# Kernel optimization log

Hardware: AMD Instinct MI355X
Metric: run time of the kernel (lower is better)

The kernel has to match this reference:

```python
import jax, jax.numpy as jnp
import numpy as np
import math

B, S, D, H, M = 2, 2048, 1024, 16, 64
HD = D // H  # head_dim = 64


def setup_inputs() -> dict:
    key = jax.random.key(0)
    ks = jax.random.split(key, 16)
    inp = {
        "query": jax.random.normal(ks[0], (B, S, D), jnp.float32),
        "key": jax.random.normal(ks[1], (B, S, D), jnp.float32),
        "value": jax.random.normal(ks[2], (B, S, D), jnp.float32),
        "mask": jax.random.randint(ks[3], (B, 1, 1, S), 0, 2, jnp.int32),
        "Wq": jax.random.normal(ks[4], (D, D), jnp.float32) * 0.02,
        "bq": jnp.zeros((D,), jnp.float32),
        "Wk": jax.random.normal(ks[5], (D, D), jnp.float32) * 0.02,
        "bk": jnp.zeros((D,), jnp.float32),
        "Wv": jax.random.normal(ks[6], (D, D), jnp.float32) * 0.02,
        "bv": jnp.zeros((D,), jnp.float32),
        "Wo": jax.random.normal(ks[7], (D, D), jnp.float32) * 0.02,
        "bo": jnp.zeros((D,), jnp.float32),
        "m_k": jax.random.normal(ks[8], (1, M, D), jnp.float32) * (1.0 / HD),
        "m_v": jax.random.normal(ks[9], (1, M, D), jnp.float32) * (1.0 / M),
    }
    return inp


def reference(query, key, value, mask, Wq, bq, Wk, bk, Wv, bv, Wo, bo, m_k, m_v):
    b, nq, d = query.shape
    nk = key.shape[1]
    h, hd, m = H, HD, M
    scale = math.sqrt(hd)

    Q = query @ Wq.T + bq                      # [b, nq, d]
    K = key @ Wk.T + bk                        # [b, nk, d]
    V = value @ Wv.T + bv                      # [b, nk, d]

    mk = scale * jnp.broadcast_to(m_k, (b, m, d))           # sqrt(head_dim)*m_k
    mv = math.sqrt(m) * jnp.broadcast_to(m_v, (b, m, d))    # sqrt(m)*m_v

    K = jnp.concatenate([K, mk], axis=1)       # [b, nk+m, d]
    V = jnp.concatenate([V, mv], axis=1)

    Qh = Q.reshape(b, nq, h, hd).transpose(0, 2, 1, 3)           # [b,h,nq,hd]
    Kh = K.reshape(b, nk + m, h, hd).transpose(0, 2, 1, 3)       # [b,h,nk+m,hd]
    Vh = V.reshape(b, nk + m, h, hd).transpose(0, 2, 1, 3)

    energy = jnp.einsum('bhqd,bhkd->bhqk', Qh, Kh) / scale       # [b,h,nq,nk+m]
    # mask only the first nk key columns; memory slots are never masked
    masked = jnp.where(mask == 0, jnp.float32(-1e20), energy[..., :nk])
    energy = jnp.concatenate([masked, energy[..., nk:]], axis=-1)

    attention = jax.nn.softmax(energy, axis=-1)
    x = jnp.einsum('bhqk,bhkd->bhqd', attention, Vh)             # [b,h,nq,hd]
    x = x.transpose(0, 2, 1, 3).reshape(b, nq, d)
    return x @ Wo.T + bo
```

## Files before the change

kernel.cpp:

```cpp
#include <hip/hip_runtime.h>
#include <hip/hip_bf16.h>
#include <stdint.h>

#define B_  2
#define S_  2048
#define D_  1024
#define H_  16
#define HD_ 64
#define M_  64
#define SKM (S_ + M_)
#define LOG2E 1.44269504088896340736f

typedef __attribute__((ext_vector_type(8))) short s16x8;
typedef __attribute__((ext_vector_type(4))) float f32x4;
typedef __attribute__((ext_vector_type(16))) float f32x16;

#define GLOAD16(gp, lp) __builtin_amdgcn_global_load_lds( \
    (const __attribute__((address_space(1))) void*)(gp),  \
    (__attribute__((address_space(3))) void*)(lp), 16, 0, 0)

#define WAITVM4() do { asm volatile("s_waitcnt vmcnt(4)" ::: "memory"); \
                       __builtin_amdgcn_sched_barrier(0); } while (0)
#define WAITVM0() do { asm volatile("s_waitcnt vmcnt(0)" ::: "memory"); \
                       __builtin_amdgcn_sched_barrier(0); } while (0)
#define BARRIER() do { asm volatile("" ::: "memory"); \
                       __builtin_amdgcn_s_barrier(); \
                       asm volatile("" ::: "memory"); } while (0)

__device__ __forceinline__ unsigned short f2bf(float f) {
  union { float f; unsigned int u; } v; v.f = f;
  unsigned int r = v.u + 0x7fffu + ((v.u >> 16) & 1u);
  return (unsigned short)(r >> 16);
}

__device__ __forceinline__ unsigned pkbf(float lo, float hi) {
  union { __hip_bfloat162 b; unsigned u; } t;
  t.b = __float22bfloat162_rn(make_float2(lo, hi));
  return t.u;
}

__global__ void compact_mask(const int* __restrict__ mask,
                             int* __restrict__ idx, int* __restrict__ cnt) {
  const int b = blockIdx.x;
  __shared__ int base, wsum[4];
  if (threadIdx.x == 0) base = 0;
  const int lane = threadIdx.x & 63, w = threadIdx.x >> 6;
  __syncthreads();
  for (int c = 0; c < S_; c += 256) {
    int key = c + threadIdx.x;
    int mv = mask[b * S_ + key];
    unsigned long long bal = __ballot(mv != 0);
    int pre = __popcll(bal & ((1ull << lane) - 1ull));
    if (lane == 0) wsum[w] = __popcll(bal);
    __syncthreads();
    int woff = 0;
    for (int i = 0; i < w; i++) woff += wsum[i];
    int tot = wsum[0] + wsum[1] + wsum[2] + wsum[3];
    if (mv) idx[b * S_ + base + woff + pre] = key;
    __syncthreads();
    if (threadIdx.x == 0) base += tot;
    __syncthreads();
  }
  if (threadIdx.x == 0) cnt[b] = base;
}

__global__ void cvt_f32_to_bf16(const float* __restrict__ in,
                                unsigned short* __restrict__ out) {
  int i = (blockIdx.x * blockDim.x + threadIdx.x) * 4;
  float4 v = *(const float4*)&in[i];
  ushort4 o;
  o.x = f2bf(v.x); o.y = f2bf(v.y); o.z = f2bf(v.z); o.w = f2bf(v.w);
  *(ushort4*)&out[i] = o;
}

__global__ void cvt_w4(const float* __restrict__ w0, const float* __restrict__ w1,
                       const float* __restrict__ w2, const float* __restrict__ w3,
                       unsigned short* __restrict__ o0, unsigned short* __restrict__ o1,
                       unsigned short* __restrict__ o2, unsigned short* __restrict__ o3) {
  const float* in; unsigned short* out;
  switch (blockIdx.y) {
    case 0: in = w0; out = o0; break;
    case 1: in = w1; out = o1; break;
    case 2: in = w2; out = o2; break;
    default: in = w3; out = o3; break;
  }
  int i = (blockIdx.x * 256 + threadIdx.x) * 4;
  float4 v = *(const float4*)&in[i];
  ushort4 o;
  o.x = f2bf(v.x); o.y = f2bf(v.y); o.z = f2bf(v.z); o.w = f2bf(v.w);
  *(ushort4*)&out[i] = o;
}

__global__ void cvt_kv_gather(const float* __restrict__ key, const float* __restrict__ value,
                              unsigned short* __restrict__ kf, unsigned short* __restrict__ vf,
                              const int* __restrict__ idx, const int* __restrict__ cnt) {
  int b = blockIdx.y, j = blockIdx.x;
  if (j >= cnt[b]) return;
  const float* in = blockIdx.z ? value : key;
  unsigned short* out = blockIdx.z ? vf : kf;
  int src = idx[b * S_ + j];
  const float* ip = in + ((size_t)(b * S_) + src) * D_;
  unsigned short* op = out + ((size_t)(b * S_) + j) * D_;
  int t = threadIdx.x * 4;
  float4 v = *(const float4*)&ip[t];
  ushort4 o;
  o.x = f2bf(v.x); o.y = f2bf(v.y); o.z = f2bf(v.z); o.w = f2bf(v.w);
  *(ushort4*)&op[t] = o;
}

__global__ void fill_mem(const float* __restrict__ mk, const float* __restrict__ mv,
                         unsigned short* __restrict__ Kb, unsigned short* __restrict__ VtG,
                         const int* __restrict__ cnt) {
  int i = blockIdx.x * 256 + threadIdx.x;
  int row = i >> 10, col = i & 1023;
  int hI = col >> 6, dd = col & 63;
  unsigned short kv = f2bf(8.0f * mk[i]);
  unsigned short vv = f2bf(8.0f * mv[i]);
#pragma unroll
  for (int b = 0; b < B_; b++) {
    int c = cnt[b];
    Kb[((size_t)(b * SKM) + c + row) * D_ + col] = kv;
    VtG[((size_t)(b * H_ + hI) * HD_ + dd) * SKM + c + row] = vv;
  }
}

__device__ __forceinline__ void gemm_core2(
    const unsigned short* __restrict__ A,
    const unsigned short* __restrict__ Bw,
    unsigned short* As, unsigned short* Bs,
    int mBase, int nBase, int K,
    int w, int lane, int wr, int wc, int lr, int lk,
    f32x4 acc[4][4]) {
  const int srow = w * 32 + (lane >> 2);
  const int cd = lane & 3;
  const int NT = K / 32;

#define STAGE_(buf, k0)                                                          \
  {                                                                              \
    _Pragma("unroll")                                                            \
    for (int i = 0; i < 2; i++) {                                                \
      int r = srow + i * 16;                                                     \
      int ca = cd ^ ((r >> 1) & 3);           \
      GLOAD16(&A[(size_t)(mBase + r) * K + (k0) + ca * 8],                       \
              &As[(buf) * (128 * 32) + (w * 32 + i * 16) * 32]);                 \
      GLOAD16(&Bw[(size_t)(nBase + r) * K + (k0) + ca * 8],                      \
              &Bs[(buf) * (128 * 32) + (w * 32 + i * 16) * 32]);                 \
    }                                                                            \
  }

  STAGE_(0, 0);
  int cur = 0;
  for (int t = 0; t < NT; ++t) {
    if (t + 1 < NT) {
      STAGE_(cur ^ 1, (t + 1) * 32);
      WAITVM4();
    } else {
      WAITVM0();
    }
    BARRIER();
    s16x8 af[4], bf[4];
#pragma unroll
    for (int mi = 0; mi < 4; mi++) {
      int row = wr * 64 + mi * 16 + lr;
      af[mi] = *(const s16x8*)&As[cur * (128 * 32) + row * 32 + ((lk ^ ((row >> 1) & 3)) << 3)];
    }
#pragma unroll
    for (int ni = 0; ni < 4; ni++) {
      int row = wc * 64 + ni * 16 + lr;
      bf[ni] = *(const s16x8*)&Bs[cur * (128 * 32) + row * 32 + ((lk ^ ((row >> 1) & 3)) << 3)];
    }
#pragma unroll
    for (int mi = 0; mi < 4; mi++)
#pragma unroll
      for (int ni = 0; ni < 4; ni++)
        acc[mi][ni] = __builtin_amdgcn_mfma_f32_16x16x32_bf16(af[mi], bf[ni], acc[mi][ni], 0, 0, 0);
    BARRIER();
    cur ^= 1;
  }
#undef STAGE_
}

__global__ __launch_bounds__(256)
void gemm_qkv(const unsigned short* __restrict__ qf, const unsigned short* __restrict__ kf,
              const unsigned short* __restrict__ vf,
              const unsigned short* __restrict__ wq, const unsigned short* __restrict__ wk,
              const unsigned short* __restrict__ wv,
              const float* __restrict__ bq, const float* __restrict__ bk,
              const float* __restrict__ bv,
              unsigned short* __restrict__ Qb, unsigned short* __restrict__ Kb,
              unsigned short* __restrict__ Vt,
              const int* __restrict__ cnt) {
  __shared__ __align__(16) unsigned short As[2 * 128 * 32];
  __shared__ __align__(16) unsigned short Bs[2 * 128 * 32];
  const int z = blockIdx.x >> 8;
  const int local = blockIdx.x & 255;
  const int ws = (local & 7) * 32 + (local >> 3);
  const int nBase = (ws & 7) * 128, mBase = (ws >> 3) * 128;
  if (z) {
    int c = (mBase < S_) ? cnt[0] : cnt[1];
    int lo = (mBase < S_) ? mBase : (mBase - S_);
    if (lo >= c) return;
  }
  const unsigned short* A  = (z == 0) ? qf : (z == 1) ? kf : vf;
  const unsigned short* Bw = (z == 0) ? wq : (z == 1) ? wk : wv;
  const float* bias        = (z == 0) ? bq : (z == 1) ? bk : bv;

  const int tid = threadIdx.x, lane = tid & 63;
  const int w = tid >> 6, wr = w >> 1, wc = w & 1;
  const int lr = lane & 15, lk = lane >> 4;

  const f32x4 fz = {0.f, 0.f, 0.f, 0.f};
  f32x4 acc[4][4];
#pragma unroll
  for (int i = 0; i < 4; i++)
#pragma unroll
    for (int j = 0; j < 4; j++) acc[i][j] = fz;

  gemm_core2(A, Bw, As, Bs, mBase, nBase, D_, w, lane, wr, wc, lr, lk, acc);

  const float alpha = (z == 0) ? 0.125f * LOG2E : 1.0f;
#pragma unroll
  for (int mi = 0; mi < 4; mi++)
#pragma unroll
    for (int ni = 0; ni < 4; ni++)
#pragma unroll
      for (int r = 0; r < 4; r++) {
        int gr = mBase + wr * 64 + mi * 16 + lk * 4 + r;
        int gc = nBase + wc * 64 + ni * 16 + lr;
        float v = (acc[mi][ni][r] + bias[gc]) * alpha;
        if (z == 2) {
          int bb = gr / S_, s = gr - bb * S_;
          int hI = gc >> 6, dd = gc & 63;
          Vt[((size_t)(bb * H_ + hI) * HD_ + dd) * SKM + s] = f2bf(v);
        } else if (z == 1) {
          int orow = gr + (gr / S_) * M_;
          Kb[(size_t)orow * D_ + gc] = f2bf(v);
        } else {
          Qb[(size_t)gr * D_ + gc] = f2bf(v);
        }
      }
}

__global__ __launch_bounds__(256)
void gemm_o(const unsigned short* __restrict__ A, const unsigned short* __restrict__ Bw,
            const float* __restrict__ bias, float* __restrict__ Cout) {
  __shared__ __align__(16) unsigned short As[2 * 128 * 32];
  __shared__ __align__(16) unsigned short Bs[2 * 128 * 32];
  const int local = blockIdx.x & 255;
  const int ws = (local & 7) * 32 + (local >> 3);
  const int nBase = (ws & 7) * 128, mBase = (ws >> 3) * 128;
  const int tid = threadIdx.x, lane = tid & 63;
  const int w = tid >> 6, wr = w >> 1, wc = w & 1;
  const int lr = lane & 15, lk = lane >> 4;

  const f32x4 fz = {0.f, 0.f, 0.f, 0.f};
  f32x4 acc[4][4];
#pragma unroll
  for (int i = 0; i < 4; i++)
#pragma unroll
    for (int j = 0; j < 4; j++) acc[i][j] = fz;

  gemm_core2(A, Bw, As, Bs, mBase, nBase, D_, w, lane, wr, wc, lr, lk, acc);

#pragma unroll
  for (int mi = 0; mi < 4; mi++)
#pragma unroll
    for (int ni = 0; ni < 4; ni++)
#pragma unroll
      for (int r = 0; r < 4; r++) {
        int gr = mBase + wr * 64 + mi * 16 + lk * 4 + r;
        int gc = nBase + wc * 64 + ni * 16 + lr;
        Cout[(size_t)gr * D_ + gc] = acc[mi][ni][r] + bias[gc];
      }
}

__global__ __launch_bounds__(512)
void attn_kernel(const unsigned short* __restrict__ Qb,
                 const unsigned short* __restrict__ Kb,
                 const unsigned short* __restrict__ VtG,
                 const int* __restrict__ cnt,
                 unsigned short* __restrict__ Xb) {
  __shared__ __align__(16) unsigned short Ks[64 * 64];
  __shared__ __align__(16) unsigned short Vs[64 * 64];

  const int tid = threadIdx.x, lane = tid & 63, w = tid >> 6;
  const int l31 = lane & 31, hh = lane >> 5;
  const int qt = blockIdx.x, h = blockIdx.y, b = blockIdx.z;

  const int total = cnt[b] + M_;
  const int nt = (total + 63) >> 6;

  const int r0 = tid >> 3, c0 = tid & 7;
  const int ck = c0 ^ (r0 & 7);
  const unsigned short* Kg = Kb + (size_t)b * SKM * D_ + (size_t)h * HD_;
  const unsigned short* Vg = VtG + (size_t)(b * H_ + h) * HD_ * SKM;

  const unsigned short* qp = Qb + ((size_t)(b * S_) + qt * 256 + w * 32 + l31) * D_ + h * HD_;
  s16x8 qf[4];
#pragma unroll
  for (int ds = 0; ds < 4; ds++) qf[ds] = *(const s16x8*)&qp[ds * 16 + hh * 8];

  f32x16 accO[2];
#pragma unroll
  for (int dt = 0; dt < 2; dt++)
#pragma unroll
    for (int j = 0; j < 16; j++) accO[dt][j] = 0.f;
  float m_r = -1e20f, l_r = 0.f;

  uint4 kr0, vr0;
  auto LOAD = [&](int kt) {
    kr0 = *(const uint4*)&Kg[(size_t)(kt * 64 + r0) * D_ + c0 * 8];
    vr0 = *(const uint4*)&Vg[(size_t)r0 * SKM + kt * 64 + c0 * 8];
  };
  LOAD(0);

  for (int kt = 0; kt < nt; ++kt) {
    __syncthreads();
    *(uint4*)&Ks[r0 * 64 + ck * 8] = kr0;
    *(uint4*)&Vs[r0 * 64 + ck * 8] = vr0;
    __syncthreads();
    if (kt + 1 < nt) LOAD(kt + 1);

    f32x16 p0, p1;
#pragma unroll
    for (int j = 0; j < 16; j++) { p0[j] = 0.f; p1[j] = 0.f; }
#pragma unroll
    for (int ds = 0; ds < 4; ds++) {
      s16x8 ka0 = *(const s16x8*)&Ks[l31 * 64 + (((ds * 2 + hh) ^ (l31 & 7)) << 3)];
      s16x8 ka1 = *(const s16x8*)&Ks[(32 + l31) * 64 + (((ds * 2 + hh) ^ (l31 & 7)) << 3)];
      p0 = __builtin_amdgcn_mfma_f32_32x32x16_bf16(ka0, qf[ds], p0, 0, 0, 0);
      p1 = __builtin_amdgcn_mfma_f32_32x32x16_bf16(ka1, qf[ds], p1, 0, 0, 0);
    }

    if (kt == nt - 1) {
      int valid = total - kt * 64;
#pragma unroll
      for (int j = 0; j < 16; j++) {
        int kl = (j & 3) + 8 * (j >> 2) + 4 * hh;
        if (kl >= valid) p0[j] = -1e30f;
        if (kl + 32 >= valid) p1[j] = -1e30f;
      }
    }

    float vmax = fmaxf(p0[0], p1[0]);
#pragma unroll
    for (int j = 1; j < 16; j++) vmax = fmaxf(vmax, fmaxf(p0[j], p1[j]));
    vmax = fmaxf(vmax, __shfl_xor(vmax, 32));
    if (!__all(vmax - m_r <= 8.0f)) {
      float mnew = fmaxf(m_r, vmax);
      float fac = __builtin_amdgcn_exp2f(m_r - mnew);
      m_r = mnew;
      l_r *= fac;
#pragma unroll
      for (int dt = 0; dt < 2; dt++)
#pragma unroll
        for (int j = 0; j < 16; j++) accO[dt][j] *= fac;
    }
    float sum = 0.f;
#pragma unroll
    for (int j = 0; j < 16; j++) {
      p0[j] = __builtin_amdgcn_exp2f(p0[j] - m_r); sum += p0[j];
      p1[j] = __builtin_amdgcn_exp2f(p1[j] - m_r); sum += p1[j];
    }
    sum += __shfl_xor(sum, 32);
    l_r += sum;

    s16x8 pf_[4];
#pragma unroll
    for (int ks = 0; ks < 4; ks++) {
      const int base = (ks & 1) * 8;
#define ELT(t) ((ks >= 2) ? p1[base + (t)] : p0[base + (t)])
      unsigned w0 = pkbf(ELT(0), ELT(1));
      unsigned w1 = pkbf(ELT(2), ELT(3));
      unsigned w2 = pkbf(ELT(4), ELT(5));
      unsigned w3 = pkbf(ELT(6), ELT(7));
#undef ELT
      unsigned s0 = hh ? w0 : w2;
      unsigned s1 = hh ? w1 : w3;
      unsigned g0 = (unsigned)__shfl_xor((int)s0, 32);
      unsigned g1 = (unsigned)__shfl_xor((int)s1, 32);
      union { s16x8 v; unsigned u[4]; } pf;
      pf.u[0] = hh ? g0 : w0;
      pf.u[1] = hh ? g1 : w1;
      pf.u[2] = hh ? w2 : g0;
      pf.u[3] = hh ? w3 : g1;
      pf_[ks] = pf.v;
    }

#pragma unroll
    for (int dt = 0; dt < 2; dt++)
#pragma unroll
      for (int ks = 0; ks < 4; ks++) {
        s16x8 va = *(const s16x8*)&Vs[(dt * 32 + l31) * 64 + (((ks * 2 + hh) ^ (l31 & 7)) << 3)];
        accO[dt] = __builtin_amdgcn_mfma_f32_32x32x16_bf16(va, pf_[ks], accO[dt], 0, 0, 0);
      }
  }

  float invl = 1.0f / l_r;
  size_t orow = ((size_t)(b * S_) + qt * 256 + w * 32 + l31) * D_ + h * HD_;
#pragma unroll
  for (int dt = 0; dt < 2; dt++)
#pragma unroll
    for (int j = 0; j < 16; j++) {
      int d = dt * 32 + (j & 3) + 8 * (j >> 2) + 4 * hh;
      Xb[orow + d] = f2bf(accO[dt][j] * invl);
    }
}

extern "C" void kernel_launch(void* const* d_in, const int* in_sizes, int n_in,
                              void* d_out, int out_size, void* d_ws, size_t ws_size,
                              hipStream_t stream) {
  const float* query = (const float*)d_in[0];
  const float* key   = (const float*)d_in[1];
  const float* value = (const float*)d_in[2];
  const int*   mask  = (const int*)d_in[3];
  const float* Wq    = (const float*)d_in[4];
  const float* bq    = (const float*)d_in[5];
  const float* Wk    = (const float*)d_in[6];
  const float* bk    = (const float*)d_in[7];
  const float* Wv    = (const float*)d_in[8];
  const float* bv    = (const float*)d_in[9];
  const float* Wo    = (const float*)d_in[10];
  const float* bo    = (const float*)d_in[11];
  const float* m_k   = (const float*)d_in[12];
  const float* m_v   = (const float*)d_in[13];

  const int NQ = B_ * S_ * D_;
  const int NW = D_ * D_;
  const int NK = B_ * SKM * D_;

  unsigned short* ws = (unsigned short*)d_ws;
  unsigned short* qf = ws;
  unsigned short* kf = qf + NQ;
  unsigned short* vf = kf + NQ;
  unsigned short* wq = vf + NQ;
  unsigned short* wk = wq + NW;
  unsigned short* wv = wk + NW;
  unsigned short* wo = wv + NW;
  unsigned short* Qb = wo + NW;
  unsigned short* Kb = Qb + NQ;
  unsigned short* Vt = Kb + NK;
  unsigned short* Xb = Vt + NK;
  int* idx = (int*)(Xb + NQ);
  int* cnt = idx + B_ * S_;

  compact_mask<<<B_, 256, 0, stream>>>(mask, idx, cnt);
  cvt_f32_to_bf16<<<NQ / 1024, 256, 0, stream>>>(query, qf);
  cvt_kv_gather<<<dim3(S_, B_, 2), 256, 0, stream>>>(key, value, kf, vf, idx, cnt);
  cvt_w4<<<dim3(NW / 1024, 4), 256, 0, stream>>>(Wq, Wk, Wv, Wo, wq, wk, wv, wo);

  gemm_qkv<<<768, 256, 0, stream>>>(qf, kf, vf, wq, wk, wv, bq, bk, bv, Qb, Kb, Vt, cnt);
  fill_mem<<<(M_ * D_) / 256, 256, 0, stream>>>(m_k, m_v, Kb, Vt, cnt);

  attn_kernel<<<dim3(S_ / 256, H_, B_), 512, 0, stream>>>(Qb, Kb, Vt, cnt, Xb);

  gemm_o<<<256, 256, 0, stream>>>(Xb, wo, bo, (float*)d_out);
}
```

Measured before the change: 133.4 us.

## Fuse fp32-to-bf16 activation conversion and masked-row gather into QKV GEMM

The separate query conversion and key/value gather-convert kernels are removed. The QKV GEMM now reads fp32 activations directly, looking up compacted row indices for K/V, converts them to bf16 in registers and writes them to LDS while the weight tiles still use direct global-to-LDS loads. This drops two kernel launches and a round trip of bf16 activations through global memory. The cost is twice the global read bytes for the A operand inside the GEMM, register-staged loads instead of async LDS loads, and full __syncthreads per iteration.

```diff
diff --git a/kernel.cpp b/kernel.cpp
--- a/kernel.cpp
+++ b/kernel.cpp
@@ -19,9 +19,7 @@
     (const __attribute__((address_space(1))) void*)(gp),  \
     (__attribute__((address_space(3))) void*)(lp), 16, 0, 0)
 
-#define WAITVM4() do { asm volatile("s_waitcnt vmcnt(4)" ::: "memory"); \
-                       __builtin_amdgcn_sched_barrier(0); } while (0)
-#define WAITVM0() do { asm volatile("s_waitcnt vmcnt(0)" ::: "memory"); \
+#define WAITVM(N) do { asm volatile("s_waitcnt vmcnt(" #N ")" ::: "memory"); \
                        __builtin_amdgcn_sched_barrier(0); } while (0)
 #define BARRIER() do { asm volatile("" ::: "memory"); \
                        __builtin_amdgcn_s_barrier(); \
@@ -64,15 +62,6 @@
   if (threadIdx.x == 0) cnt[b] = base;
 }
 
-__global__ void cvt_f32_to_bf16(const float* __restrict__ in,
-                                unsigned short* __restrict__ out) {
-  int i = (blockIdx.x * blockDim.x + threadIdx.x) * 4;
-  float4 v = *(const float4*)&in[i];
-  ushort4 o;
-  o.x = f2bf(v.x); o.y = f2bf(v.y); o.z = f2bf(v.z); o.w = f2bf(v.w);
-  *(ushort4*)&out[i] = o;
-}
-
 __global__ void cvt_w4(const float* __restrict__ w0, const float* __restrict__ w1,
                        const float* __restrict__ w2, const float* __restrict__ w3,
                        unsigned short* __restrict__ o0, unsigned short* __restrict__ o1,
@@ -91,23 +80,6 @@
   *(ushort4*)&out[i] = o;
 }
 
-__global__ void cvt_kv_gather(const float* __restrict__ key, const float* __restrict__ value,
-                              unsigned short* __restrict__ kf, unsigned short* __restrict__ vf,
-                              const int* __restrict__ idx, const int* __restrict__ cnt) {
-  int b = blockIdx.y, j = blockIdx.x;
-  if (j >= cnt[b]) return;
-  const float* in = blockIdx.z ? value : key;
-  unsigned short* out = blockIdx.z ? vf : kf;
-  int src = idx[b * S_ + j];
-  const float* ip = in + ((size_t)(b * S_) + src) * D_;
-  unsigned short* op = out + ((size_t)(b * S_) + j) * D_;
-  int t = threadIdx.x * 4;
-  float4 v = *(const float4*)&ip[t];
-  ushort4 o;
-  o.x = f2bf(v.x); o.y = f2bf(v.y); o.z = f2bf(v.z); o.w = f2bf(v.w);
-  *(ushort4*)&op[t] = o;
-}
-
 __global__ void fill_mem(const float* __restrict__ mk, const float* __restrict__ mv,
                          unsigned short* __restrict__ Kb, unsigned short* __restrict__ VtG,
                          const int* __restrict__ cnt) {
@@ -140,7 +112,7 @@
     _Pragma("unroll")                                                            \
     for (int i = 0; i < 2; i++) {                                                \
       int r = srow + i * 16;                                                     \
-      int ca = cd ^ ((r >> 1) & 3);           \
+      int ca = cd ^ ((r >> 1) & 3);                                              \
       GLOAD16(&A[(size_t)(mBase + r) * K + (k0) + ca * 8],                       \
               &As[(buf) * (128 * 32) + (w * 32 + i * 16) * 32]);                 \
       GLOAD16(&Bw[(size_t)(nBase + r) * K + (k0) + ca * 8],                      \
@@ -153,9 +125,9 @@
   for (int t = 0; t < NT; ++t) {
     if (t + 1 < NT) {
       STAGE_(cur ^ 1, (t + 1) * 32);
-      WAITVM4();
+      WAITVM(4);
     } else {
-      WAITVM0();
+      WAITVM(0);
     }
     BARRIER();
     s16x8 af[4], bf[4];
@@ -181,33 +153,52 @@
 }
 
 __global__ __launch_bounds__(256)
-void gemm_qkv(const unsigned short* __restrict__ qf, const unsigned short* __restrict__ kf,
-              const unsigned short* __restrict__ vf,
+void gemm_qkv(const float* __restrict__ query, const float* __restrict__ key,
+              const float* __restrict__ value,
               const unsigned short* __restrict__ wq, const unsigned short* __restrict__ wk,
               const unsigned short* __restrict__ wv,
               const float* __restrict__ bq, const float* __restrict__ bk,
               const float* __restrict__ bv,
               unsigned short* __restrict__ Qb, unsigned short* __restrict__ Kb,
               unsigned short* __restrict__ Vt,
-              const int* __restrict__ cnt) {
+              const int* __restrict__ idx, const int* __restrict__ cnt) {
   __shared__ __align__(16) unsigned short As[2 * 128 * 32];
   __shared__ __align__(16) unsigned short Bs[2 * 128 * 32];
   const int z = blockIdx.x >> 8;
   const int local = blockIdx.x & 255;
-  const int ws = (local & 7) * 32 + (local >> 3);
-  const int nBase = (ws & 7) * 128, mBase = (ws >> 3) * 128;
+  const int wsz = (local & 7) * 32 + (local >> 3);
+  const int nBase = (wsz & 7) * 128, mBase = (wsz >> 3) * 128;
+  const int bb = (mBase >= S_);
   if (z) {
-    int c = (mBase < S_) ? cnt[0] : cnt[1];
-    int lo = (mBase < S_) ? mBase : (mBase - S_);
-    if (lo >= c) return;
-  }
-  const unsigned short* A  = (z == 0) ? qf : (z == 1) ? kf : vf;
+    if (mBase - bb * S_ >= cnt[bb]) return;
+  }
+  const float* Af          = (z == 0) ? query : (z == 1) ? key : value;
   const unsigned short* Bw = (z == 0) ? wq : (z == 1) ? wk : wv;
   const float* bias        = (z == 0) ? bq : (z == 1) ? bk : bv;
 
   const int tid = threadIdx.x, lane = tid & 63;
   const int w = tid >> 6, wr = w >> 1, wc = w & 1;
   const int lr = lane & 15, lk = lane >> 4;
+  const int srow = w * 32 + (lane >> 2);
+  const int cd = lane & 3;
+
+  size_t rb0, rb1;
+  {
+    int cb = z ? cnt[bb] : 0;
+    int r0g = mBase + srow, r1g = mBase + srow + 16;
+    if (z == 0) { rb0 = (size_t)r0g * D_; rb1 = (size_t)r1g * D_; }
+    else {
+      int j0 = r0g - bb * S_, j1 = r1g - bb * S_;
+      int s0 = (j0 < cb) ? idx[bb * S_ + j0] : 0;
+      int s1 = (j1 < cb) ? idx[bb * S_ + j1] : 0;
+      rb0 = ((size_t)(bb * S_) + s0) * D_;
+      rb1 = ((size_t)(bb * S_) + s1) * D_;
+    }
+  }
+  const int dA0 = srow * 32 + ((cd ^ ((srow >> 1) & 3)) << 3);
+  const int dA1 = (srow + 16) * 32 + ((cd ^ (((srow + 16) >> 1) & 3)) << 3);
+  const int caB0 = cd ^ ((srow >> 1) & 3);
+  const int caB1 = cd ^ (((srow + 16) >> 1) & 3);
 
   const f32x4 fz = {0.f, 0.f, 0.f, 0.f};
   f32x4 acc[4][4];
@@ -216,7 +207,62 @@
 #pragma unroll
     for (int j = 0; j < 4; j++) acc[i][j] = fz;
 
-  gemm_core2(A, Bw, As, Bs, mBase, nBase, D_, w, lane, wr, wc, lr, lk, acc);
+  const int NT = D_ / 32;
+
+  {
+    float4 a0l = *(const float4*)&Af[rb0 + cd * 8];
+    float4 a0h = *(const float4*)&Af[rb0 + cd * 8 + 4];
+    float4 a1l = *(const float4*)&Af[rb1 + cd * 8];
+    float4 a1h = *(const float4*)&Af[rb1 + cd * 8 + 4];
+    GLOAD16(&Bw[(size_t)(nBase + srow) * D_ + caB0 * 8], &Bs[(w * 32) * 32]);
+    GLOAD16(&Bw[(size_t)(nBase + srow + 16) * D_ + caB1 * 8], &Bs[(w * 32 + 16) * 32]);
+    uint4 w0 = { pkbf(a0l.x, a0l.y), pkbf(a0l.z, a0l.w), pkbf(a0h.x, a0h.y), pkbf(a0h.z, a0h.w) };
+    uint4 w1 = { pkbf(a1l.x, a1l.y), pkbf(a1l.z, a1l.w), pkbf(a1h.x, a1h.y), pkbf(a1h.z, a1h.w) };
+    *(uint4*)&As[dA0] = w0;
+    *(uint4*)&As[dA1] = w1;
+  }
+  __syncthreads();
+
+  int cur = 0;
+  for (int t = 0; t < NT; ++t) {
+    float4 a0l, a0h, a1l, a1h;
+    const bool pre = (t + 1 < NT);
+    if (pre) {
+      const int k1 = (t + 1) * 32;
+      a0l = *(const float4*)&Af[rb0 + k1 + cd * 8];
+      a0h = *(const float4*)&Af[rb0 + k1 + cd * 8 + 4];
+      a1l = *(const float4*)&Af[rb1 + k1 + cd * 8];
+      a1h = *(const float4*)&Af[rb1 + k1 + cd * 8 + 4];
+      GLOAD16(&Bw[(size_t)(nBase + srow) * D_ + k1 + caB0 * 8],
+              &Bs[(cur ^ 1) * (128 * 32) + (w * 32) * 32]);
+      GLOAD16(&Bw[(size_t)(nBase + srow + 16) * D_ + k1 + caB1 * 8],
+              &Bs[(cur ^ 1) * (128 * 32) + (w * 32 + 16) * 32]);
+    }
+    s16x8 af[4], bf[4];
+#pragma unroll
+    for (int mi = 0; mi < 4; mi++) {
+      int row = wr * 64 + mi * 16 + lr;
+      af[mi] = *(const s16x8*)&As[cur * (128 * 32) + row * 32 + ((lk ^ ((row >> 1) & 3)) << 3)];
+    }
+#pragma unroll
+    for (int ni = 0; ni < 4; ni++) {
+      int row = wc * 64 + ni * 16 + lr;
+      bf[ni] = *(const s16x8*)&Bs[cur * (128 * 32) + row * 32 + ((lk ^ ((row >> 1) & 3)) << 3)];
+    }
+#pragma unroll
+    for (int mi = 0; mi < 4; mi++)
+#pragma unroll
+      for (int ni = 0; ni < 4; ni++)
+        acc[mi][ni] = __builtin_amdgcn_mfma_f32_16x16x32_bf16(af[mi], bf[ni], acc[mi][ni], 0, 0, 0);
+    if (pre) {
+      uint4 w0 = { pkbf(a0l.x, a0l.y), pkbf(a0l.z, a0l.w), pkbf(a0h.x, a0h.y), pkbf(a0h.z, a0h.w) };
+      uint4 w1 = { pkbf(a1l.x, a1l.y), pkbf(a1l.z, a1l.w), pkbf(a1h.x, a1h.y), pkbf(a1h.z, a1h.w) };
+      *(uint4*)&As[(cur ^ 1) * (128 * 32) + dA0] = w0;
+      *(uint4*)&As[(cur ^ 1) * (128 * 32) + dA1] = w1;
+    }
+    __syncthreads();
+    cur ^= 1;
+  }
 
   const float alpha = (z == 0) ? 0.125f * LOG2E : 1.0f;
 #pragma unroll
@@ -229,11 +275,11 @@
         int gc = nBase + wc * 64 + ni * 16 + lr;
         float v = (acc[mi][ni][r] + bias[gc]) * alpha;
         if (z == 2) {
-          int bb = gr / S_, s = gr - bb * S_;
+          int s = gr - bb * S_;
           int hI = gc >> 6, dd = gc & 63;
           Vt[((size_t)(bb * H_ + hI) * HD_ + dd) * SKM + s] = f2bf(v);
         } else if (z == 1) {
-          int orow = gr + (gr / S_) * M_;
+          int orow = gr + bb * M_;
           Kb[(size_t)orow * D_ + gc] = f2bf(v);
         } else {
           Qb[(size_t)gr * D_ + gc] = f2bf(v);
@@ -247,8 +293,8 @@
   __shared__ __align__(16) unsigned short As[2 * 128 * 32];
   __shared__ __align__(16) unsigned short Bs[2 * 128 * 32];
   const int local = blockIdx.x & 255;
-  const int ws = (local & 7) * 32 + (local >> 3);
-  const int nBase = (ws & 7) * 128, mBase = (ws >> 3) * 128;
+  const int wsz = (local & 7) * 32 + (local >> 3);
+  const int nBase = (wsz & 7) * 128, mBase = (wsz >> 3) * 128;
   const int tid = threadIdx.x, lane = tid & 63;
   const int w = tid >> 6, wr = w >> 1, wc = w & 1;
   const int lr = lane & 15, lk = lane >> 4;
@@ -430,10 +476,7 @@
   const int NK = B_ * SKM * D_;
 
   unsigned short* ws = (unsigned short*)d_ws;
-  unsigned short* qf = ws;
-  unsigned short* kf = qf + NQ;
-  unsigned short* vf = kf + NQ;
-  unsigned short* wq = vf + NQ;
+  unsigned short* wq = ws;
   unsigned short* wk = wq + NW;
   unsigned short* wv = wk + NW;
   unsigned short* wo = wv + NW;
@@ -445,11 +488,10 @@
   int* cnt = idx + B_ * S_;
 
   compact_mask<<<B_, 256, 0, stream>>>(mask, idx, cnt);
-  cvt_f32_to_bf16<<<NQ / 1024, 256, 0, stream>>>(query, qf);
-  cvt_kv_gather<<<dim3(S_, B_, 2), 256, 0, stream>>>(key, value, kf, vf, idx, cnt);
   cvt_w4<<<dim3(NW / 1024, 4), 256, 0, stream>>>(Wq, Wk, Wv, Wo, wq, wk, wv, wo);
 
-  gemm_qkv<<<768, 256, 0, stream>>>(qf, kf, vf, wq, wk, wv, bq, bk, bv, Qb, Kb, Vt, cnt);
+  gemm_qkv<<<768, 256, 0, stream>>>(query, key, value, wq, wk, wv,
+                                    bq, bk, bv, Qb, Kb, Vt, idx, cnt);
   fill_mem<<<(M_ * D_) / 256, 256, 0, stream>>>(m_k, m_v, Kb, Vt, cnt);
 
   attn_kernel<<<dim3(S_ / 256, H_, B_), 512, 0, stream>>>(Qb, Kb, Vt, cnt, Xb);
```

After: 134.3 us. No clear change (+0.6%).
